# Kernel tuning notes

Measured on AMD Instinct MI355X. Metric: run time of the kernel, lower is better.

## Reference

```python
import jax, jax.numpy as jnp
import numpy as np

EPS = 1e-8

def div_small(a, b):
    b_safe = b * (b > EPS) + (b <= EPS) * EPS
    return a / b_safe

def cos_full(q1h, q2h, w):
    # q1h [b,s1,h], q2h [b,s1_or_1,h], w [P,h] -> [b,s1,P]
    a = q1h[:, :, None, :] * w          # [b,s1,P,h]
    c = q2h[:, :, None, :] * w          # [b,s1|1,P,h]
    num = jnp.sum(a * c, axis=-1)
    den = jnp.maximum(jnp.linalg.norm(a, axis=-1) * jnp.linalg.norm(c, axis=-1), EPS)
    return num / den

def cos_maxpool(q1h, q2h, w):
    # q1h [b,s1,h], q2h [b,s2,h], w [P,h] -> max over s2 of cosine -> [b,s1,P]
    a = q1h[:, :, None, :] * w          # [b,s1,P,h]
    c = q2h[:, :, None, :] * w          # [b,s2,P,h]
    num = jnp.einsum('biph,bjph->bijp', a, c)            # [b,s1,s2,P]
    na = jnp.linalg.norm(a, axis=-1)                     # [b,s1,P]
    nc = jnp.linalg.norm(c, axis=-1)                     # [b,s2,P]
    den = jnp.maximum(na[:, :, None, :] * nc[:, None, :, :], EPS)
    return jnp.max(num / den, axis=2)

def attention(q1, q2):
    # cosine-similarity matrix [b,s1,s2]
    n1 = jnp.linalg.norm(q1, axis=2, keepdims=True)      # [b,s1,1]
    n2 = jnp.linalg.norm(q2, axis=2, keepdims=True)      # [b,s2,1]
    num = jnp.einsum('bih,bjh->bij', q1, q2)
    return div_small(num, n1 * jnp.swapaxes(n2, 1, 2))

def setup_inputs() -> dict:
    key = jax.random.key(0)
    k1, k2, kw = jax.random.split(key, 3)
    q1_batch = jax.random.normal(k1, (16, 128, 512), dtype=jnp.float32)
    q2_batch = jax.random.normal(k2, (16, 128, 512), dtype=jnp.float32)
    W = jax.random.normal(kw, (8, 16, 256), dtype=jnp.float32)
    return {"q1_batch": q1_batch, "q2_batch": q2_batch, "W": W}

def reference(q1_batch, q2_batch, W):
    h = q1_batch.shape[-1] // 2
    q1_fw, q1_bw = q1_batch[..., :h], q1_batch[..., h:]
    q2_fw, q2_bw = q2_batch[..., :h], q2_batch[..., h:]

    # 1) full matching against last (fw) / first (bw) q2 state
    full_fw = cos_full(q1_fw, q2_fw[:, -1:, :], W[0])
    full_bw = cos_full(q1_bw, q2_bw[:, :1, :], W[1])

    # 2) max-pool matching over all q2 positions
    max_fw = cos_maxpool(q1_fw, q2_fw, W[2])
    max_bw = cos_maxpool(q1_bw, q2_bw, W[3])

    # 3) attentive matching
    att_fw = attention(q1_fw, q2_fw)                     # [b,s1,s2]
    att_bw = attention(q1_bw, q2_bw)
    at_q2_fw = att_fw[..., None] * q2_fw[:, None, :, :]  # [b,s1,s2,h]
    at_q2_bw = att_bw[..., None] * q2_bw[:, None, :, :]
    mean_fw = div_small(at_q2_fw.sum(axis=2), att_fw.sum(axis=2, keepdims=True))
    # NOTE: denominator intentionally uses att_fw (bug preserved from source)
    mean_bw = div_small(at_q2_bw.sum(axis=2), att_fw.sum(axis=2, keepdims=True))
    attn_fw = cos_full(q1_fw, mean_fw, W[4])
    attn_bw = cos_full(q1_bw, mean_bw, W[5])

    # 4) max-attentive matching
    max_at_fw = at_q2_fw.max(axis=2)                     # [b,s1,h]
    max_at_bw = at_q2_bw.max(axis=2)
    maxattn_fw = cos_full(q1_fw, max_at_fw, W[6])
    maxattn_bw = cos_full(q1_bw, max_at_bw, W[7])

    return jnp.concatenate(
        [full_fw, full_bw, max_fw, max_bw, attn_fw, attn_bw, maxattn_fw, maxattn_bw],
        axis=-1)
```

## Files before the change

### kernel.cpp

```cpp
#include <hip/hip_runtime.h>
#include <hip/hip_bf16.h>

#define B 16
#define L 128
#define H 256
#define H2 512
#define P 16
#define EPSF 1e-8f
#define LDSTR 72

typedef __attribute__((ext_vector_type(8))) short short8;
typedef __attribute__((ext_vector_type(4))) short short4v;
typedef __attribute__((ext_vector_type(4))) float f32x4;

__device__ __forceinline__ short f2bf(float x) {
    unsigned u = __builtin_bit_cast(unsigned, x);
    u += 0x7fffu + ((u >> 16) & 1u);
    return (short)(u >> 16);
}
__device__ __forceinline__ float bf2f(short s) {
    unsigned u = ((unsigned)(unsigned short)s) << 16;
    return __builtin_bit_cast(float, u);
}

__global__ void __launch_bounds__(256) k_att_mfma(
        const float* __restrict__ q1, const float* __restrict__ q2,
        float* __restrict__ att_fw, float* __restrict__ att_bw,
        float* __restrict__ attsum) {
    int bd = blockIdx.x;
    int b = bd >> 1, dir = bd & 1;
    int m0 = blockIdx.y * 16;
    int t = threadIdx.x;

    __shared__ short As[16 * LDSTR];
    __shared__ short Bs[128 * LDSTR];
    __shared__ float nA[16], nB[L];
    __shared__ float part[4][16];

    f32x4 acc[2];
    acc[0] = (f32x4){0.f, 0.f, 0.f, 0.f};
    acc[1] = (f32x4){0.f, 0.f, 0.f, 0.f};

    int wave = t >> 6;
    int l = t & 63;
    int q = l >> 4;
    int coll = l & 15;
    int n0 = wave * 32;

    int arow = t >> 4;
    int acol = (t & 15) * 4;
    int brow = t >> 1;
    int bcol0 = (t & 1) * 32;

    const float* q1b = q1 + ((size_t)b * L + m0) * H2 + dir * H;
    const float* q2b = q2 + ((size_t)b * L) * H2 + dir * H;

    float normA = 0.f, normB = 0.f;

    for (int kt = 0; kt < 4; kt++) {
        int k0 = kt * 64;
        {
            float4 va = *(const float4*)(q1b + (size_t)arow * H2 + k0 + acol);
            normA += va.x * va.x + va.y * va.y + va.z * va.z + va.w * va.w;
            short4v sa = { f2bf(va.x), f2bf(va.y), f2bf(va.z), f2bf(va.w) };
            *(short4v*)(As + arow * LDSTR + acol) = sa;
        }
        for (int cc = 0; cc < 8; cc++) {
            float4 vb = *(const float4*)(q2b + (size_t)brow * H2 + k0 + bcol0 + cc * 4);
            normB += vb.x * vb.x + vb.y * vb.y + vb.z * vb.z + vb.w * vb.w;
            short4v sb = { f2bf(vb.x), f2bf(vb.y), f2bf(vb.z), f2bf(vb.w) };
            *(short4v*)(Bs + brow * LDSTR + bcol0 + cc * 4) = sb;
        }
        __syncthreads();
        for (int ks = 0; ks < 2; ks++) {
            int koff = ks * 32 + q * 8;
            short8 af = *(const short8*)(As + coll * LDSTR + koff);
            short8 bf0 = *(const short8*)(Bs + (n0 + coll) * LDSTR + koff);
            short8 bf1 = *(const short8*)(Bs + (n0 + 16 + coll) * LDSTR + koff);
            acc[0] = __builtin_amdgcn_mfma_f32_16x16x32_bf16(af, bf0, acc[0], 0, 0, 0);
            acc[1] = __builtin_amdgcn_mfma_f32_16x16x32_bf16(af, bf1, acc[1], 0, 0, 0);
        }
        __syncthreads();
    }
    {
        float sA = normA;
        for (int off = 1; off < 16; off <<= 1) sA += __shfl_xor(sA, off, 16);
        if ((t & 15) == 0) nA[arow] = sqrtf(sA);
        float sB = normB + __shfl_xor(normB, 1, 2);
        if ((t & 1) == 0) nB[brow] = sqrtf(sB);
    }
    __syncthreads();

    float* attout = dir ? att_bw : att_fw;
    size_t bL = (size_t)b * L;
    float n1v[4];
    for (int r = 0; r < 4; r++) n1v[r] = nA[q * 4 + r];
    float rsum[4] = {0.f, 0.f, 0.f, 0.f};
    for (int nt = 0; nt < 2; nt++) {
        int col = n0 + nt * 16 + coll;
        float n2v = nB[col];
        for (int r = 0; r < 4; r++) {
            int row = m0 + q * 4 + r;
            float den = n1v[r] * n2v;
            den = den > EPSF ? den : EPSF;
            float a = acc[nt][r] / den;
            attout[(bL + row) * L + col] = a;
            rsum[r] += a;
        }
    }
    if (dir == 0) {
        for (int off = 1; off < 16; off <<= 1)
            for (int r = 0; r < 4; r++)
                rsum[r] += __shfl_xor(rsum[r], off, 16);
        if (coll == 0)
            for (int r = 0; r < 4; r++)
                part[wave][q * 4 + r] = rsum[r];
        __syncthreads();
        if (t < 16)
            attsum[bL + m0 + t] = part[0][t] + part[1][t] + part[2][t] + part[3][t];
    }
}

__global__ void __launch_bounds__(256) k_meanmax_v2(
        const float* __restrict__ q2,
        const float* __restrict__ att_fw, const float* __restrict__ att_bw,
        const float* __restrict__ attsum,
        float* __restrict__ mean_fw, float* __restrict__ mean_bw,
        float* __restrict__ maxat_fw, float* __restrict__ maxat_bw) {
    int bd = blockIdx.x;
    int b = bd >> 1, dir = bd & 1;
    int i0 = blockIdx.y * 8;
    int t = threadIdx.x;
    int wave = t >> 6, l = t & 63;

    __shared__ float at[8][L];
    __shared__ float Ss[8];
    __shared__ f32x4 red[4][64][4];

    const float* att = dir ? att_bw : att_fw;
    for (int v = t; v < 8 * L; v += 256) {
        int r = v >> 7, j = v & 127;
        at[r][j] = att[((size_t)b * L + i0 + r) * L + j];
    }
    if (t < 8) {
        float s = attsum[(size_t)b * L + i0 + t];
        Ss[t] = s > EPSF ? s : EPSF;
    }
    __syncthreads();

    f32x4 sum[8], mx[8];
    for (int r = 0; r < 8; r++) {
        sum[r] = (f32x4){0.f, 0.f, 0.f, 0.f};
        mx[r] = (f32x4){-INFINITY, -INFINITY, -INFINITY, -INFINITY};
    }

    const float* q2b = q2 + (size_t)b * L * H2 + dir * H;
    for (int jj = 0; jj < 32; jj++) {
        int j = wave * 32 + jj;
        float4 c = *(const float4*)(q2b + (size_t)j * H2 + l * 4);
        for (int r = 0; r < 8; r++) {
            float w = at[r][j];
            f32x4 v = { w * c.x, w * c.y, w * c.z, w * c.w };
            sum[r] += v;
            mx[r][0] = fmaxf(mx[r][0], v[0]);
            mx[r][1] = fmaxf(mx[r][1], v[1]);
            mx[r][2] = fmaxf(mx[r][2], v[2]);
            mx[r][3] = fmaxf(mx[r][3], v[3]);
        }
    }

    float* meanout = dir ? mean_bw : mean_fw;
    float* maxout = dir ? maxat_bw : maxat_fw;
    for (int rr = 0; rr < 4; rr++) {
        __syncthreads();
        red[wave][l][0] = sum[rr * 2];
        red[wave][l][1] = mx[rr * 2];
        red[wave][l][2] = sum[rr * 2 + 1];
        red[wave][l][3] = mx[rr * 2 + 1];
        __syncthreads();
        if (t < 128) {
            int r2 = t >> 6;
            int lane = t & 63;
            f32x4 s = red[0][lane][r2 * 2];
            f32x4 m = red[0][lane][r2 * 2 + 1];
            for (int w = 1; w < 4; w++) {
                s += red[w][lane][r2 * 2];
                f32x4 m2 = red[w][lane][r2 * 2 + 1];
                m[0] = fmaxf(m[0], m2[0]);
                m[1] = fmaxf(m[1], m2[1]);
                m[2] = fmaxf(m[2], m2[2]);
                m[3] = fmaxf(m[3], m2[3]);
            }
            int row = i0 + rr * 2 + r2;
            float inv = 1.f / Ss[rr * 2 + r2];
            size_t o = ((size_t)b * L + row) * H + lane * 4;
            *(f32x4*)(meanout + o) = s * inv;
            *(f32x4*)(maxout + o) = m;
        }
    }
}

__global__ void __launch_bounds__(256) k_cosfull(
        const float* __restrict__ q1, const float* __restrict__ q2,
        const float* __restrict__ mean_fw, const float* __restrict__ mean_bw,
        const float* __restrict__ maxat_fw, const float* __restrict__ maxat_bw,
        const float* __restrict__ W, float* __restrict__ out) {
    int blk = blockIdx.x;
    int piece = blockIdx.y;
    int b = blk / L;
    int t = threadIdx.x;
    int p = t >> 4, l = t & 15;

    int widx, col, dir;
    const float* vptr;
    switch (piece) {
        case 0: widx = 0; col = 0;   dir = 0; vptr = q2 + ((size_t)b * L + (L - 1)) * H2;  break;
        case 1: widx = 1; col = 16;  dir = 1; vptr = q2 + ((size_t)b * L) * H2 + H;        break;
        case 2: widx = 4; col = 64;  dir = 0; vptr = mean_fw + (size_t)blk * H;            break;
        case 3: widx = 5; col = 80;  dir = 1; vptr = mean_bw + (size_t)blk * H;            break;
        case 4: widx = 6; col = 96;  dir = 0; vptr = maxat_fw + (size_t)blk * H;           break;
        default: widx = 7; col = 112; dir = 1; vptr = maxat_bw + (size_t)blk * H;          break;
    }
    const float* r1 = q1 + (size_t)blk * H2 + dir * H;
    const float* wrow = W + ((size_t)widx * P + p) * H;
    float num = 0, na = 0, nc = 0;
    for (int k = 0; k < 16; k++) {
        int h = l + 16 * k;
        float wv = wrow[h];
        float ws = wv * wv;
        float a = r1[h];
        float c = vptr[h];
        num += a * c * ws;
        na  += a * a * ws;
        nc  += c * c * ws;
    }
    for (int off = 8; off; off >>= 1) {
        num += __shfl_down(num, off, 16);
        na  += __shfl_down(na,  off, 16);
        nc  += __shfl_down(nc,  off, 16);
    }
    if (l == 0) {
        float den = sqrtf(na) * sqrtf(nc);
        den = den > EPSF ? den : EPSF;
        out[(size_t)blk * 128 + col + p] = num / den;
    }
}

__global__ void __launch_bounds__(256, 2) k_maxpool_mfma(
        const float* __restrict__ q1, const float* __restrict__ q2,
        const float* __restrict__ W, float* __restrict__ out) {
    int bd = blockIdx.x;
    int b = bd >> 1, dir = bd & 1;
    int p = blockIdx.y;
    int t = threadIdx.x;

    __shared__ short As[128 * LDSTR];
    __shared__ short Bs[128 * LDSTR];
    __shared__ float wv[H];
    __shared__ float nrm[256];

    wv[t] = W[((size_t)(2 + dir) * P + p) * H + t];
    __syncthreads();

    f32x4 acc[2][8];
    for (int mt = 0; mt < 2; mt++)
        for (int nt = 0; nt < 8; nt++)
            acc[mt][nt] = (f32x4){0.f, 0.f, 0.f, 0.f};

    int lane16 = t & 15;
    int rgrp = t >> 4;
    int nrow = t & 127;
    int nmat = t >> 7;
    float normacc = 0.f;

    int wave = t >> 6;
    int l = t & 63;
    int q = l >> 4;
    int coll = l & 15;
    int m0 = wave * 32;

    const float* q1b = q1 + ((size_t)b * L) * H2 + dir * H;
    const float* q2b = q2 + ((size_t)b * L) * H2 + dir * H;

    for (int kt = 0; kt < 4; kt++) {
        int k0 = kt * 64;
        for (int pass = 0; pass < 8; pass++) {
            int row = rgrp + pass * 16;
            int c4 = lane16 * 4;
            float w0 = wv[k0 + c4], w1 = wv[k0 + c4 + 1];
            float w2 = wv[k0 + c4 + 2], w3 = wv[k0 + c4 + 3];
            float4 va = *(const float4*)(q1b + (size_t)row * H2 + k0 + c4);
            short4v sa = { f2bf(va.x * w0), f2bf(va.y * w1), f2bf(va.z * w2), f2bf(va.w * w3) };
            *(short4v*)(As + row * LDSTR + c4) = sa;
            float4 vb = *(const float4*)(q2b + (size_t)row * H2 + k0 + c4);
            short4v sb = { f2bf(vb.x * w0), f2bf(vb.y * w1), f2bf(vb.z * w2), f2bf(vb.w * w3) };
            *(short4v*)(Bs + row * LDSTR + c4) = sb;
        }
        __syncthreads();
        {
            const short* rowp = (nmat ? Bs : As) + nrow * LDSTR;
            for (int c = 0; c < 8; c++) {
                short8 s = *(const short8*)(rowp + c * 8);
                for (int jj = 0; jj < 8; jj++) {
                    float f = bf2f(s[jj]);
                    normacc += f * f;
                }
            }
        }
        for (int ks = 0; ks < 2; ks++) {
            int koff = ks * 32 + q * 8;
            short8 af0 = *(const short8*)(As + (m0 + coll) * LDSTR + koff);
            short8 af1 = *(const short8*)(As + (m0 + 16 + coll) * LDSTR + koff);
            for (int nt = 0; nt < 8; nt++) {
                short8 bfr = *(const short8*)(Bs + (nt * 16 + coll) * LDSTR + koff);
                acc[0][nt] = __builtin_amdgcn_mfma_f32_16x16x32_bf16(af0, bfr, acc[0][nt], 0, 0, 0);
                acc[1][nt] = __builtin_amdgcn_mfma_f32_16x16x32_bf16(af1, bfr, acc[1][nt], 0, 0, 0);
            }
        }
        __syncthreads();
    }
    nrm[t] = sqrtf(normacc);
    __syncthreads();

    float nav[2][4];
    for (int mt = 0; mt < 2; mt++)
        for (int r = 0; r < 4; r++)
            nav[mt][r] = nrm[m0 + mt * 16 + q * 4 + r];
    float rmax[2][4];
    for (int mt = 0; mt < 2; mt++)
        for (int r = 0; r < 4; r++) rmax[mt][r] = -INFINITY;
    for (int nt = 0; nt < 8; nt++) {
        float ncv = nrm[128 + nt * 16 + coll];
        for (int mt = 0; mt < 2; mt++)
            for (int r = 0; r < 4; r++) {
                float den = fmaxf(nav[mt][r] * ncv, EPSF);
                float v = acc[mt][nt][r] / den;
                rmax[mt][r] = fmaxf(rmax[mt][r], v);
            }
    }
    for (int off = 1; off < 16; off <<= 1)
        for (int mt = 0; mt < 2; mt++)
            for (int r = 0; r < 4; r++)
                rmax[mt][r] = fmaxf(rmax[mt][r], __shfl_xor(rmax[mt][r], off, 16));
    if (coll == 0) {
        for (int mt = 0; mt < 2; mt++)
            for (int r = 0; r < 4; r++) {
                int row = m0 + mt * 16 + q * 4 + r;
                out[((size_t)b * L + row) * 128 + 32 + dir * 16 + p] = rmax[mt][r];
            }
    }
}

extern "C" void kernel_launch(void* const* d_in, const int* in_sizes, int n_in,
                              void* d_out, int out_size, void* d_ws, size_t ws_size,
                              hipStream_t stream) {
    const float* q1 = (const float*)d_in[0];
    const float* q2 = (const float*)d_in[1];
    const float* W  = (const float*)d_in[2];
    float* out = (float*)d_out;

    float* ws = (float*)d_ws;
    float* attsum = ws;
    float* att_fw = attsum + B * L;
    float* att_bw = att_fw + (size_t)B * L * L;
    float* mean_fw = att_bw + (size_t)B * L * L;
    float* mean_bw = mean_fw + (size_t)B * L * H;
    float* maxat_fw = mean_bw + (size_t)B * L * H;
    float* maxat_bw = maxat_fw + (size_t)B * L * H;

    k_att_mfma<<<dim3(B * 2, 8), 256, 0, stream>>>(q1, q2, att_fw, att_bw, attsum);
    k_meanmax_v2<<<dim3(B * 2, 16), 256, 0, stream>>>(q2, att_fw, att_bw, attsum,
                                                      mean_fw, mean_bw, maxat_fw, maxat_bw);
    k_cosfull<<<dim3(B * L, 6), 256, 0, stream>>>(q1, q2, mean_fw, mean_bw,
                                                  maxat_fw, maxat_bw, W, out);
    k_maxpool_mfma<<<dim3(B * 2, P), 256, 0, stream>>>(q1, q2, W, out);
}
```

Measured before the change: 128.6 us.

## Fuse attention, mean/max pooling and cosine matching into one kernel

Merges the attention MFMA kernel, the mean/max-attentive reduction kernel and the full-cosine kernel into one 512-thread kernel. The attention tile, the pooled mean/max vectors and the matching outputs now stay in LDS instead of passing through global workspace buffers. The division by the attention row sum is dropped because cosine similarity is unchanged by a positive scale. This removes two launches and the global writes and reads of the intermediates. In exchange each block carries more LDS and more serial work, and each block rereads all of q2 for its 16 rows.

```diff
diff --git a/kernel.cpp b/kernel.cpp
--- a/kernel.cpp
+++ b/kernel.cpp
@@ -8,6 +8,8 @@
 #define P 16
 #define EPSF 1e-8f
 #define LDSTR 72
+#define PADQ 260
+#define PATT 132
 
 typedef __attribute__((ext_vector_type(8))) short short8;
 typedef __attribute__((ext_vector_type(4))) short short4v;
@@ -23,226 +25,143 @@
     return __builtin_bit_cast(float, u);
 }
 
-__global__ void __launch_bounds__(256) k_att_mfma(
+__global__ void __launch_bounds__(512) k_fused(
         const float* __restrict__ q1, const float* __restrict__ q2,
-        float* __restrict__ att_fw, float* __restrict__ att_bw,
-        float* __restrict__ attsum) {
+        const float* __restrict__ W, float* __restrict__ out) {
     int bd = blockIdx.x;
     int b = bd >> 1, dir = bd & 1;
     int m0 = blockIdx.y * 16;
     int t = threadIdx.x;
-
-    __shared__ short As[16 * LDSTR];
-    __shared__ short Bs[128 * LDSTR];
-    __shared__ float nA[16], nB[L];
-    __shared__ float part[4][16];
-
-    f32x4 acc[2];
-    acc[0] = (f32x4){0.f, 0.f, 0.f, 0.f};
-    acc[1] = (f32x4){0.f, 0.f, 0.f, 0.f};
-
-    int wave = t >> 6;
-    int l = t & 63;
-    int q = l >> 4;
-    int coll = l & 15;
-    int n0 = wave * 32;
-
-    int arow = t >> 4;
-    int acol = (t & 15) * 4;
-    int brow = t >> 1;
-    int bcol0 = (t & 1) * 32;
+    int wave = t >> 6, l = t & 63, q = l >> 4, coll = l & 15;
+
+    __shared__ __align__(16) short As[16 * LDSTR];
+    __shared__ __align__(16) short Bs[128 * LDSTR];
+    __shared__ __align__(16) float att_s[16][PATT];
+    __shared__ __align__(16) float meanS[16][PADQ];
+    __shared__ __align__(16) float maxS[16][PADQ];
+    __shared__ __align__(16) float cful[256];
+    __shared__ float nA[16], nB[128];
 
     const float* q1b = q1 + ((size_t)b * L + m0) * H2 + dir * H;
-    const float* q2b = q2 + ((size_t)b * L) * H2 + dir * H;
-
+    const float* q2b = q2 + (size_t)b * L * H2 + dir * H;
+
+    f32x4 acc = (f32x4){0.f, 0.f, 0.f, 0.f};
     float normA = 0.f, normB = 0.f;
+    int arow = t >> 4, acol = (t & 15) * 4;
+    int brow = t >> 2, bc0 = (t & 3) * 16;
 
     for (int kt = 0; kt < 4; kt++) {
         int k0 = kt * 64;
-        {
+        if (t < 256) {
             float4 va = *(const float4*)(q1b + (size_t)arow * H2 + k0 + acol);
             normA += va.x * va.x + va.y * va.y + va.z * va.z + va.w * va.w;
             short4v sa = { f2bf(va.x), f2bf(va.y), f2bf(va.z), f2bf(va.w) };
             *(short4v*)(As + arow * LDSTR + acol) = sa;
         }
-        for (int cc = 0; cc < 8; cc++) {
-            float4 vb = *(const float4*)(q2b + (size_t)brow * H2 + k0 + bcol0 + cc * 4);
+        for (int cc = 0; cc < 4; cc++) {
+            float4 vb = *(const float4*)(q2b + (size_t)brow * H2 + k0 + bc0 + cc * 4);
             normB += vb.x * vb.x + vb.y * vb.y + vb.z * vb.z + vb.w * vb.w;
             short4v sb = { f2bf(vb.x), f2bf(vb.y), f2bf(vb.z), f2bf(vb.w) };
-            *(short4v*)(Bs + brow * LDSTR + bcol0 + cc * 4) = sb;
+            *(short4v*)(Bs + brow * LDSTR + bc0 + cc * 4) = sb;
         }
         __syncthreads();
         for (int ks = 0; ks < 2; ks++) {
             int koff = ks * 32 + q * 8;
             short8 af = *(const short8*)(As + coll * LDSTR + koff);
-            short8 bf0 = *(const short8*)(Bs + (n0 + coll) * LDSTR + koff);
-            short8 bf1 = *(const short8*)(Bs + (n0 + 16 + coll) * LDSTR + koff);
-            acc[0] = __builtin_amdgcn_mfma_f32_16x16x32_bf16(af, bf0, acc[0], 0, 0, 0);
-            acc[1] = __builtin_amdgcn_mfma_f32_16x16x32_bf16(af, bf1, acc[1], 0, 0, 0);
-        }
-        __syncthreads();
-    }
-    {
+            short8 bf = *(const short8*)(Bs + (wave * 16 + coll) * LDSTR + koff);
+            acc = __builtin_amdgcn_mfma_f32_16x16x32_bf16(af, bf, acc, 0, 0, 0);
+        }
+        __syncthreads();
+    }
+    if (t < 256) {
         float sA = normA;
         for (int off = 1; off < 16; off <<= 1) sA += __shfl_xor(sA, off, 16);
         if ((t & 15) == 0) nA[arow] = sqrtf(sA);
-        float sB = normB + __shfl_xor(normB, 1, 2);
-        if ((t & 1) == 0) nB[brow] = sqrtf(sB);
-    }
-    __syncthreads();
-
-    float* attout = dir ? att_bw : att_fw;
-    size_t bL = (size_t)b * L;
-    float n1v[4];
-    for (int r = 0; r < 4; r++) n1v[r] = nA[q * 4 + r];
-    float rsum[4] = {0.f, 0.f, 0.f, 0.f};
-    for (int nt = 0; nt < 2; nt++) {
-        int col = n0 + nt * 16 + coll;
-        float n2v = nB[col];
+    }
+    {
+        float sB = normB;
+        sB += __shfl_xor(sB, 1, 4);
+        sB += __shfl_xor(sB, 2, 4);
+        if ((t & 3) == 0) nB[brow] = sqrtf(sB);
+    }
+    __syncthreads();
+    {
+        float n2 = nB[wave * 16 + coll];
         for (int r = 0; r < 4; r++) {
-            int row = m0 + q * 4 + r;
-            float den = n1v[r] * n2v;
+            float den = nA[q * 4 + r] * n2;
             den = den > EPSF ? den : EPSF;
-            float a = acc[nt][r] / den;
-            attout[(bL + row) * L + col] = a;
-            rsum[r] += a;
-        }
-    }
-    if (dir == 0) {
-        for (int off = 1; off < 16; off <<= 1)
-            for (int r = 0; r < 4; r++)
-                rsum[r] += __shfl_xor(rsum[r], off, 16);
-        if (coll == 0)
-            for (int r = 0; r < 4; r++)
-                part[wave][q * 4 + r] = rsum[r];
-        __syncthreads();
-        if (t < 16)
-            attsum[bL + m0 + t] = part[0][t] + part[1][t] + part[2][t] + part[3][t];
-    }
-}
-
-__global__ void __launch_bounds__(256) k_meanmax_v2(
-        const float* __restrict__ q2,
-        const float* __restrict__ att_fw, const float* __restrict__ att_bw,
-        const float* __restrict__ attsum,
-        float* __restrict__ mean_fw, float* __restrict__ mean_bw,
-        float* __restrict__ maxat_fw, float* __restrict__ maxat_bw) {
-    int bd = blockIdx.x;
-    int b = bd >> 1, dir = bd & 1;
-    int i0 = blockIdx.y * 8;
-    int t = threadIdx.x;
-    int wave = t >> 6, l = t & 63;
-
-    __shared__ float at[8][L];
-    __shared__ float Ss[8];
-    __shared__ f32x4 red[4][64][4];
-
-    const float* att = dir ? att_bw : att_fw;
-    for (int v = t; v < 8 * L; v += 256) {
-        int r = v >> 7, j = v & 127;
-        at[r][j] = att[((size_t)b * L + i0 + r) * L + j];
-    }
-    if (t < 8) {
-        float s = attsum[(size_t)b * L + i0 + t];
-        Ss[t] = s > EPSF ? s : EPSF;
-    }
-    __syncthreads();
-
-    f32x4 sum[8], mx[8];
-    for (int r = 0; r < 8; r++) {
-        sum[r] = (f32x4){0.f, 0.f, 0.f, 0.f};
-        mx[r] = (f32x4){-INFINITY, -INFINITY, -INFINITY, -INFINITY};
-    }
-
-    const float* q2b = q2 + (size_t)b * L * H2 + dir * H;
-    for (int jj = 0; jj < 32; jj++) {
-        int j = wave * 32 + jj;
-        float4 c = *(const float4*)(q2b + (size_t)j * H2 + l * 4);
-        for (int r = 0; r < 8; r++) {
-            float w = at[r][j];
-            f32x4 v = { w * c.x, w * c.y, w * c.z, w * c.w };
-            sum[r] += v;
-            mx[r][0] = fmaxf(mx[r][0], v[0]);
-            mx[r][1] = fmaxf(mx[r][1], v[1]);
-            mx[r][2] = fmaxf(mx[r][2], v[2]);
-            mx[r][3] = fmaxf(mx[r][3], v[3]);
-        }
-    }
-
-    float* meanout = dir ? mean_bw : mean_fw;
-    float* maxout = dir ? maxat_bw : maxat_fw;
-    for (int rr = 0; rr < 4; rr++) {
-        __syncthreads();
-        red[wave][l][0] = sum[rr * 2];
-        red[wave][l][1] = mx[rr * 2];
-        red[wave][l][2] = sum[rr * 2 + 1];
-        red[wave][l][3] = mx[rr * 2 + 1];
-        __syncthreads();
-        if (t < 128) {
-            int r2 = t >> 6;
-            int lane = t & 63;
-            f32x4 s = red[0][lane][r2 * 2];
-            f32x4 m = red[0][lane][r2 * 2 + 1];
-            for (int w = 1; w < 4; w++) {
-                s += red[w][lane][r2 * 2];
-                f32x4 m2 = red[w][lane][r2 * 2 + 1];
-                m[0] = fmaxf(m[0], m2[0]);
-                m[1] = fmaxf(m[1], m2[1]);
-                m[2] = fmaxf(m[2], m2[2]);
-                m[3] = fmaxf(m[3], m2[3]);
-            }
-            int row = i0 + rr * 2 + r2;
-            float inv = 1.f / Ss[rr * 2 + r2];
-            size_t o = ((size_t)b * L + row) * H + lane * 4;
-            *(f32x4*)(meanout + o) = s * inv;
-            *(f32x4*)(maxout + o) = m;
-        }
-    }
-}
-
-__global__ void __launch_bounds__(256) k_cosfull(
-        const float* __restrict__ q1, const float* __restrict__ q2,
-        const float* __restrict__ mean_fw, const float* __restrict__ mean_bw,
-        const float* __restrict__ maxat_fw, const float* __restrict__ maxat_bw,
-        const float* __restrict__ W, float* __restrict__ out) {
-    int blk = blockIdx.x;
-    int piece = blockIdx.y;
-    int b = blk / L;
-    int t = threadIdx.x;
-    int p = t >> 4, l = t & 15;
-
-    int widx, col, dir;
-    const float* vptr;
-    switch (piece) {
-        case 0: widx = 0; col = 0;   dir = 0; vptr = q2 + ((size_t)b * L + (L - 1)) * H2;  break;
-        case 1: widx = 1; col = 16;  dir = 1; vptr = q2 + ((size_t)b * L) * H2 + H;        break;
-        case 2: widx = 4; col = 64;  dir = 0; vptr = mean_fw + (size_t)blk * H;            break;
-        case 3: widx = 5; col = 80;  dir = 1; vptr = mean_bw + (size_t)blk * H;            break;
-        case 4: widx = 6; col = 96;  dir = 0; vptr = maxat_fw + (size_t)blk * H;           break;
-        default: widx = 7; col = 112; dir = 1; vptr = maxat_bw + (size_t)blk * H;          break;
-    }
-    const float* r1 = q1 + (size_t)blk * H2 + dir * H;
-    const float* wrow = W + ((size_t)widx * P + p) * H;
-    float num = 0, na = 0, nc = 0;
-    for (int k = 0; k < 16; k++) {
-        int h = l + 16 * k;
-        float wv = wrow[h];
-        float ws = wv * wv;
-        float a = r1[h];
-        float c = vptr[h];
-        num += a * c * ws;
-        na  += a * a * ws;
-        nc  += c * c * ws;
-    }
-    for (int off = 8; off; off >>= 1) {
-        num += __shfl_down(num, off, 16);
-        na  += __shfl_down(na,  off, 16);
-        nc  += __shfl_down(nc,  off, 16);
-    }
-    if (l == 0) {
-        float den = sqrtf(na) * sqrtf(nc);
-        den = den > EPSF ? den : EPSF;
-        out[(size_t)blk * 128 + col + p] = num / den;
+            att_s[q * 4 + r][wave * 16 + coll] = acc[r] / den;
+        }
+    }
+    if (t < 256) cful[t] = q2b[(size_t)(dir ? 0 : (L - 1)) * H2 + t];
+    __syncthreads();
+
+    int ig = t >> 6, hq = t & 63;
+    int ia = ig * 2, ib = ia + 1;
+    f32x4 s0 = (f32x4){0.f, 0.f, 0.f, 0.f}, s1 = s0;
+    f32x4 mx0 = (f32x4){-INFINITY, -INFINITY, -INFINITY, -INFINITY}, mx1 = mx0;
+    for (int j = 0; j < 128; j += 2) {
+        float4 c0 = *(const float4*)(q2b + (size_t)j * H2 + hq * 4);
+        float4 c1 = *(const float4*)(q2b + (size_t)(j + 1) * H2 + hq * 4);
+        float wa0 = att_s[ia][j],     wb0 = att_s[ib][j];
+        float wa1 = att_s[ia][j + 1], wb1 = att_s[ib][j + 1];
+        f32x4 v0 = (f32x4){ wa0 * c0.x, wa0 * c0.y, wa0 * c0.z, wa0 * c0.w };
+        f32x4 v1 = (f32x4){ wb0 * c0.x, wb0 * c0.y, wb0 * c0.z, wb0 * c0.w };
+        f32x4 v2 = (f32x4){ wa1 * c1.x, wa1 * c1.y, wa1 * c1.z, wa1 * c1.w };
+        f32x4 v3 = (f32x4){ wb1 * c1.x, wb1 * c1.y, wb1 * c1.z, wb1 * c1.w };
+        s0 += v0; s0 += v2;
+        s1 += v1; s1 += v3;
+        mx0[0] = fmaxf(mx0[0], fmaxf(v0[0], v2[0]));
+        mx0[1] = fmaxf(mx0[1], fmaxf(v0[1], v2[1]));
+        mx0[2] = fmaxf(mx0[2], fmaxf(v0[2], v2[2]));
+        mx0[3] = fmaxf(mx0[3], fmaxf(v0[3], v2[3]));
+        mx1[0] = fmaxf(mx1[0], fmaxf(v1[0], v3[0]));
+        mx1[1] = fmaxf(mx1[1], fmaxf(v1[1], v3[1]));
+        mx1[2] = fmaxf(mx1[2], fmaxf(v1[2], v3[2]));
+        mx1[3] = fmaxf(mx1[3], fmaxf(v1[3], v3[3]));
+    }
+    *(f32x4*)&meanS[ia][hq * 4] = s0;
+    *(f32x4*)&meanS[ib][hq * 4] = s1;
+    *(f32x4*)&maxS[ia][hq * 4] = mx0;
+    *(f32x4*)&maxS[ib][hq * 4] = mx1;
+    __syncthreads();
+
+    int p3 = t >> 5, i3 = (t >> 1) & 15, half = t & 1;
+    const float* a3 = q1b + (size_t)i3 * H2;
+    for (int pc = 0; pc < 3; pc++) {
+        int widx = (pc == 0) ? dir : (pc == 1 ? 4 + dir : 6 + dir);
+        const float* crow = (pc == 0) ? cful : (pc == 1 ? &meanS[i3][0] : &maxS[i3][0]);
+        const float* wg = W + (size_t)widx * 4096 + p3 * 256;
+        float num = 0.f, na = 0.f, nc = 0.f;
+        for (int ch = 0; ch < 32; ch++) {
+            int h = half * 128 + ch * 4;
+            float4 a4 = *(const float4*)(a3 + h);
+            f32x4 c4 = *(const f32x4*)(crow + h);
+            float4 w4 = *(const float4*)(wg + h);
+            float ws0 = w4.x * w4.x, ws1 = w4.y * w4.y;
+            float ws2 = w4.z * w4.z, ws3 = w4.w * w4.w;
+            num += a4.x * c4[0] * ws0;
+            na  += a4.x * a4.x * ws0;
+            nc  += c4[0] * c4[0] * ws0;
+            num += a4.y * c4[1] * ws1;
+            na  += a4.y * a4.y * ws1;
+            nc  += c4[1] * c4[1] * ws1;
+            num += a4.z * c4[2] * ws2;
+            na  += a4.z * a4.z * ws2;
+            nc  += c4[2] * c4[2] * ws2;
+            num += a4.w * c4[3] * ws3;
+            na  += a4.w * a4.w * ws3;
+            nc  += c4[3] * c4[3] * ws3;
+        }
+        num += __shfl_xor(num, 1, 2);
+        na  += __shfl_xor(na, 1, 2);
+        nc  += __shfl_xor(nc, 1, 2);
+        if (half == 0) {
+            float den = sqrtf(na) * sqrtf(nc);
+            den = den > EPSF ? den : EPSF;
+            int colbase = (pc == 0 ? 0 : pc == 1 ? 64 : 96) + dir * 16;
+            out[((size_t)b * L + m0 + i3) * 128 + colbase + p3] = num / den;
+        }
     }
 }
 
@@ -254,8 +173,8 @@
     int p = blockIdx.y;
     int t = threadIdx.x;
 
-    __shared__ short As[128 * LDSTR];
-    __shared__ short Bs[128 * LDSTR];
+    __shared__ __align__(16) short As[128 * LDSTR];
+    __shared__ __align__(16) short Bs[128 * LDSTR];
     __shared__ float wv[H];
     __shared__ float nrm[256];
 
@@ -358,20 +277,8 @@
     const float* q2 = (const float*)d_in[1];
     const float* W  = (const float*)d_in[2];
     float* out = (float*)d_out;
-
-    float* ws = (float*)d_ws;
-    float* attsum = ws;
-    float* att_fw = attsum + B * L;
-    float* att_bw = att_fw + (size_t)B * L * L;
-    float* mean_fw = att_bw + (size_t)B * L * L;
-    float* mean_bw = mean_fw + (size_t)B * L * H;
-    float* maxat_fw = mean_bw + (size_t)B * L * H;
-    float* maxat_bw = maxat_fw + (size_t)B * L * H;
-
-    k_att_mfma<<<dim3(B * 2, 8), 256, 0, stream>>>(q1, q2, att_fw, att_bw, attsum);
-    k_meanmax_v2<<<dim3(B * 2, 16), 256, 0, stream>>>(q2, att_fw, att_bw, attsum,
-                                                      mean_fw, mean_bw, maxat_fw, maxat_bw);
-    k_cosfull<<<dim3(B * L, 6), 256, 0, stream>>>(q1, q2, mean_fw, mean_bw,
-                                                  maxat_fw, maxat_bw, W, out);
+    (void)d_ws; (void)ws_size;
+
+    k_fused<<<dim3(B * 2, 8), 512, 0, stream>>>(q1, q2, W, out);
     k_maxpool_mfma<<<dim3(B * 2, P), 256, 0, stream>>>(q1, q2, W, out);
 }
```

Result: no change. 126.9 us (-1.3%).
